# Kernel optimization log

Measured on AMD Instinct MI355X. Metric: run time of the kernel, lower is better.

## Reference

```python
import jax, jax.numpy as jnp
import numpy as np

H = 4  # num_heads


def _ln(x, g, b, eps=1e-5):
    m = x.mean(-1, keepdims=True)
    v = ((x - m) ** 2).mean(-1, keepdims=True)
    return (x - m) / jnp.sqrt(v + eps) * g + b


def setup_inputs() -> dict:
    key = jax.random.key(0)
    ks = jax.random.split(key, 16)
    B, N, M, dQ, dK, dV = 4, 2048, 2048, 128, 128, 128
    s = 0.02
    return {
        "Q": jax.random.normal(ks[0], (B, N, dQ), jnp.float32),
        "K": jax.random.normal(ks[1], (B, M, dK), jnp.float32),
        "adj_mask": jax.random.randint(ks[2], (B, N, M), 0, 2, jnp.int32),
        "Wq": jax.random.normal(ks[3], (dQ, dV), jnp.float32) * s,
        "bq": jnp.zeros((dV,), jnp.float32),
        "Wk": jax.random.normal(ks[4], (dK, dV), jnp.float32) * s,
        "bk": jnp.zeros((dV,), jnp.float32),
        "Wv": jax.random.normal(ks[5], (dK, dV), jnp.float32) * s,
        "bv": jnp.zeros((dV,), jnp.float32),
        "Wr1": jax.random.normal(ks[6], (dV, dV), jnp.float32) * s,
        "br1": jnp.zeros((dV,), jnp.float32),
        "Wr2": jax.random.normal(ks[7], (dV, dV), jnp.float32) * s,
        "br2": jnp.zeros((dV,), jnp.float32),
        "g0": jnp.ones((dV,), jnp.float32),
        "be0": jnp.zeros((dV,), jnp.float32),
        "g1": jnp.ones((dV,), jnp.float32),
        "be1": jnp.zeros((dV,), jnp.float32),
    }


def reference(Q, K, adj_mask, Wq, bq, Wk, bk, Wv, bv, Wr1, br1, Wr2, br2, g0, be0, g1, be1):
    B, N, _ = Q.shape
    M = K.shape[1]
    dV = Wq.shape[1]
    dh = dV // H
    Qp = Q @ Wq + bq   # [B,N,dV]
    Kp = K @ Wk + bk   # [B,M,dV]
    Vp = K @ Wv + bv   # [B,M,dV]
    # torch: split dim_V into H chunks, cat along dim 0 -> head-major [H*B, L, dh]
    def to_heads(x, L):
        return x.reshape(B, L, H, dh).transpose(2, 0, 1, 3).reshape(H * B, L, dh)
    Qh, Kh, Vh = to_heads(Qp, N), to_heads(Kp, M), to_heads(Vp, M)
    attn = jnp.einsum('bnd,bmd->bnm', Qh, Kh) / jnp.sqrt(jnp.float32(dh))  # [H*B,N,M]
    # torch repeat_interleave(mask, H, dim=0) gives batch-major order -- faithful
    mask = jnp.repeat(adj_mask, H, axis=0)
    attn = jnp.where(mask == 0, -jnp.inf, attn)
    A = jax.nn.softmax(attn, axis=2)
    O = Qh + jnp.einsum('bnm,bmd->bnd', A, Vh)  # [H*B,N,dh]
    # recombine heads back to [B,N,dV] (intended split(dim=0)/cat(dim=2))
    O = O.reshape(H, B, N, dh).transpose(1, 2, 0, 3).reshape(B, N, dV)
    O = _ln(O, g0, be0)
    O = O + (jax.nn.relu(O @ Wr1 + br1) @ Wr2 + br2)
    return _ln(O, g1, be1)
```

## Files before the change

kernel.cpp:

```cpp
#include <hip/hip_runtime.h>
#include <hip/hip_bf16.h>


typedef short bf16x8 __attribute__((ext_vector_type(8)));
typedef float f32x4 __attribute__((ext_vector_type(4)));

#define BN 4
#define SEQ 2048
#define DIM 128
#define NH 4
#define DH 32
#define ROWS (BN * SEQ)
#define MS 4

static __device__ __forceinline__ unsigned short f2bf(float f) {
    __hip_bfloat16 h = __float2bfloat16(f);
    return *reinterpret_cast<unsigned short*>(&h);
}
static __device__ __forceinline__ float bf2f(unsigned short u) {
    union { unsigned int i; float f; } cv;
    cv.i = ((unsigned int)u) << 16;
    return cv.f;
}
static __device__ __forceinline__ unsigned int pack2bf(float a, float b) {
    return (unsigned int)f2bf(a) | ((unsigned int)f2bf(b) << 16);
}

__global__ __launch_bounds__(256) void proj_prep(
    const float* __restrict__ Q, const float* __restrict__ K,
    const float* __restrict__ bq, const float* __restrict__ bk,
    const float* __restrict__ bv,
    const float* __restrict__ Wq, const float* __restrict__ Wk,
    const float* __restrict__ Wv, const float* __restrict__ W1,
    const float* __restrict__ W2,
    float* __restrict__ Qp, unsigned short* __restrict__ Qb,
    unsigned short* __restrict__ Kb, unsigned short* __restrict__ Vt,
    unsigned short* __restrict__ WT)
{
    __shared__ __align__(16) unsigned char smem[52288];
    const int bx = blockIdx.x;
    const int t = threadIdx.x;

    if (bx >= 768) {
        const float* W = (bx == 768) ? W1 : W2;
        unsigned short* out = WT + (bx - 768) * DIM * DIM;
        for (int i = t; i < DIM * DIM; i += 256) {
            int n = i >> 7, k = i & 127;
            out[i] = f2bf(W[k * DIM + n]);
        }
        return;
    }

    unsigned short (*sW)[136] = (unsigned short(*)[136])smem;
    unsigned short (*sX)[136] = (unsigned short(*)[136])(smem + 34816);
    unsigned short (*sY)[137] = (unsigned short(*)[137])(smem + 43520);

    const int proj = bx >> 8;
    const int rowbase = (bx & 255) * 32;
    const float* X = (proj == 0) ? Q : K;
    const float* W = (proj == 0) ? Wq : (proj == 1) ? Wk : Wv;
    const float* bias = (proj == 0) ? bq : (proj == 1) ? bk : bv;
    const int bidx = rowbase >> 11;
    const int srowbase = rowbase & 2047;

#pragma unroll
    for (int i = 0; i < 16; ++i) {
        int idx = i * 256 + t;
        int k = idx >> 5, n4 = (idx & 31) * 4;
        float4 v = *(const float4*)(W + k * DIM + n4);
        sW[n4 + 0][k] = f2bf(v.x);
        sW[n4 + 1][k] = f2bf(v.y);
        sW[n4 + 2][k] = f2bf(v.z);
        sW[n4 + 3][k] = f2bf(v.w);
    }
#pragma unroll
    for (int i = 0; i < 4; ++i) {
        int idx = i * 256 + t;
        int row = idx >> 5, c4 = (idx & 31) * 4;
        float4 v = *(const float4*)(X + (long)(rowbase + row) * DIM + c4);
        sX[row][c4 + 0] = f2bf(v.x);
        sX[row][c4 + 1] = f2bf(v.y);
        sX[row][c4 + 2] = f2bf(v.z);
        sX[row][c4 + 3] = f2bf(v.w);
    }
    __syncthreads();

    const int w = t >> 6, lane = t & 63;
    const int n16 = lane & 15, quad = lane >> 4;

    f32x4 acc[2][2];
#pragma unroll
    for (int r = 0; r < 2; ++r)
#pragma unroll
        for (int ct = 0; ct < 2; ++ct)
            acc[r][ct] = (f32x4){0.f, 0.f, 0.f, 0.f};

    for (int ks = 0; ks < 4; ++ks) {
        bf16x8 bfrag[2];
#pragma unroll
        for (int ct = 0; ct < 2; ++ct) {
            int ncol = w * 32 + ct * 16 + n16;
            bfrag[ct] = *(const bf16x8*)(&sW[ncol][ks * 32 + quad * 8]);
        }
#pragma unroll
        for (int r = 0; r < 2; ++r) {
            bf16x8 afrag = *(const bf16x8*)(&sX[r * 16 + n16][ks * 32 + quad * 8]);
#pragma unroll
            for (int ct = 0; ct < 2; ++ct)
                acc[r][ct] = __builtin_amdgcn_mfma_f32_16x16x32_bf16(
                    afrag, bfrag[ct], acc[r][ct], 0, 0, 0);
        }
    }

#pragma unroll
    for (int r = 0; r < 2; ++r) {
#pragma unroll
        for (int ct = 0; ct < 2; ++ct) {
            int col = w * 32 + ct * 16 + n16;
            int hh = col >> 5, dd = col & 31;
            float bv_ = bias[col];
#pragma unroll
            for (int i = 0; i < 4; ++i) {
                int lrow = r * 16 + quad * 4 + i;
                int grow = rowbase + lrow;
                int srow = srowbase + lrow;
                float val = acc[r][ct][i] + bv_;
                if (proj == 0) {
                    Qp[(long)grow * DIM + col] = val;
                    Qb[((long)(hh * BN + bidx) * SEQ + srow) * DH + dd]
                        = f2bf(val * 0.17677669529663687f);
                } else if (proj == 1) {
                    Kb[((long)(hh * BN + bidx) * SEQ + srow) * DH + dd] = f2bf(val);
                } else {
                    sY[lrow][col] = f2bf(val);
                }
            }
        }
    }
    if (proj == 2) {
        __syncthreads();
#pragma unroll
        for (int i = 0; i < 16; ++i) {
            int idx = i * 256 + t;
            int c = idx >> 5, m = idx & 31;
            Vt[((long)bidx * DIM + c) * SEQ + srowbase + m] = sY[m][c];
        }
    }
}

__global__ __launch_bounds__(256, 2) void attn_kernel(
    const unsigned short* __restrict__ Qb, const unsigned short* __restrict__ Kb,
    const unsigned short* __restrict__ Vt, const int* __restrict__ adj,
    unsigned short* __restrict__ Opart, float* __restrict__ Lpart)
{
    __shared__ __align__(16) unsigned short sP[4][32][68];

    const int id = blockIdx.x;
    const int combo = id & 15;
    const int qidx = id >> 4;
    const int h = combo >> 2;
    const int sp = combo & 3;
    const int qbase = qidx * 32;
    const int t = threadIdx.x;
    const int b = t >> 6;
    const int lane = t & 63, n16 = lane & 15, quad = lane >> 4;

    const unsigned short* Qh = Qb + ((long)(h * BN + b) * SEQ) * DH + quad * 8;
    const unsigned short* Kp = Kb + ((long)(h * BN + b) * SEQ) * DH + quad * 8;
    const unsigned short* Vp = Vt + ((long)b * DIM + h * DH) * SEQ + quad * 8;
    const int* Mr[2];
#pragma unroll
    for (int r = 0; r < 2; ++r)
        Mr[r] = adj + ((long)h * SEQ + qbase + r * 16 + n16) * SEQ + quad * 4;

    bf16x8 qfrag[2];
#pragma unroll
    for (int r = 0; r < 2; ++r)
        qfrag[r] = *(const bf16x8*)(Qh + (long)(qbase + r * 16 + n16) * DH);

    f32x4 o[2][2];
    float lsum[2];
#pragma unroll
    for (int r = 0; r < 2; ++r) {
#pragma unroll
        for (int ct = 0; ct < 2; ++ct) o[r][ct] = (f32x4){0.f, 0.f, 0.f, 0.f};
        lsum[r] = 0.f;
    }

    bf16x8 kf[2][2];
    int4 mk[2][2][2];
    const int mb0 = sp * 512;

#pragma unroll
    for (int c = 0; c < 2; ++c)
        kf[0][c] = *(const bf16x8*)(Kp + (long)(mb0 + c * 16 + n16) * DH);
#pragma unroll
    for (int r = 0; r < 2; ++r)
#pragma unroll
        for (int c = 0; c < 2; ++c)
            mk[0][r][c] = *(const int4*)(Mr[r] + mb0 + c * 16);

    const f32x4 zero4 = {0.f, 0.f, 0.f, 0.f};

#pragma unroll
    for (int mt = 0; mt < 16; ++mt) {
        const int cur = mt & 1, nxt = cur ^ 1;
        const int mbc = mb0 + mt * 32;
        bf16x8 vf0 = *(const bf16x8*)(Vp + (long)(0 * 16 + n16) * SEQ + mbc);
        bf16x8 vf1 = *(const bf16x8*)(Vp + (long)(1 * 16 + n16) * SEQ + mbc);
        if (mt < 15) {
            const int mb = mbc + 32;
#pragma unroll
            for (int c = 0; c < 2; ++c)
                kf[nxt][c] = *(const bf16x8*)(Kp + (long)(mb + c * 16 + n16) * DH);
#pragma unroll
            for (int r = 0; r < 2; ++r)
#pragma unroll
                for (int c = 0; c < 2; ++c)
                    mk[nxt][r][c] = *(const int4*)(Mr[r] + mb + c * 16);
        }
#pragma unroll
        for (int r = 0; r < 2; ++r) {
            f32x4 st[2];
#pragma unroll
            for (int c = 0; c < 2; ++c)
                st[c] = __builtin_amdgcn_mfma_f32_16x16x32_bf16(
                    kf[cur][c], qfrag[r], zero4, 0, 0, 0);
            float p[2][4];
#pragma unroll
            for (int c = 0; c < 2; ++c) {
                const int* mp = (const int*)&mk[cur][r][c];
#pragma unroll
                for (int i = 0; i < 4; ++i) {
                    float e = __expf(st[c][i]);
                    p[c][i] = mp[i] ? e : 0.f;
                    lsum[r] += p[c][i];
                }
            }
#pragma unroll
            for (int c = 0; c < 2; ++c) {
                uint2 wv;
                wv.x = pack2bf(p[c][0], p[c][1]);
                wv.y = pack2bf(p[c][2], p[c][3]);
                *(uint2*)&sP[b][r * 16 + n16][c * 16 + quad * 4] = wv;
            }
        }
#pragma unroll
        for (int r = 0; r < 2; ++r) {
            bf16x8 pa = *(const bf16x8*)(&sP[b][r * 16 + n16][quad * 8]);
            o[r][0] = __builtin_amdgcn_mfma_f32_16x16x32_bf16(pa, vf0, o[r][0], 0, 0, 0);
            o[r][1] = __builtin_amdgcn_mfma_f32_16x16x32_bf16(pa, vf1, o[r][1], 0, 0, 0);
        }
    }

#pragma unroll
    for (int r = 0; r < 2; ++r) {
        lsum[r] += __shfl_xor(lsum[r], 16, 64);
        lsum[r] += __shfl_xor(lsum[r], 32, 64);
    }

#pragma unroll
    for (int r = 0; r < 2; ++r)
#pragma unroll
        for (int ct = 0; ct < 2; ++ct)
#pragma unroll
            for (int i = 0; i < 4; ++i)
                sP[b][r * 16 + quad * 4 + i][ct * 16 + n16] = f2bf(o[r][ct][i]);
    {
        const uint4 w0 = *(const uint4*)&sP[b][lane >> 1][(lane & 1) * 16];
        const uint4 w1 = *(const uint4*)&sP[b][lane >> 1][(lane & 1) * 16 + 8];
        unsigned short* Ob = Opart
            + ((((long)sp * NH + h) * BN + b) * SEQ + qbase) * 32;
        *(uint4*)(Ob + (long)lane * 16)     = w0;
        *(uint4*)(Ob + (long)lane * 16 + 8) = w1;
    }

    if (quad == 0) {
#pragma unroll
        for (int r = 0; r < 2; ++r)
            Lpart[(((long)sp * BN + b) * NH + h) * SEQ + qbase + r * 16 + n16] = lsum[r];
    }
}

__global__ __launch_bounds__(256) void epi_kernel(
    const float* __restrict__ Qp, const unsigned short* __restrict__ Opart,
    const float* __restrict__ Lpart, const unsigned short* __restrict__ WT,
    const float* __restrict__ br1, const float* __restrict__ br2,
    const float* __restrict__ g0, const float* __restrict__ be0,
    const float* __restrict__ g1, const float* __restrict__ be1,
    float* __restrict__ out)
{
    __shared__ __align__(16) unsigned short sXb[16][136];
    __shared__ __align__(16) unsigned short sHb[16][136];
    __shared__ __align__(16) float sXf[16][132];

    const int rowbase = blockIdx.x * 16;
    const int t = threadIdx.x;
    const int row = t >> 4, col8 = (t & 15) * 8;
    const int grow = rowbase + row;
    const int bidx = grow >> 11;
    const int srow = grow & 2047;
    const int head = col8 >> 5;
    const int dd = col8 & 31;

    {
        float l = 0.f;
#pragma unroll
        for (int s = 0; s < MS; ++s)
            l += Lpart[(((long)s * BN + bidx) * NH + head) * SEQ + srow];
        float linv = 1.f / l;

        float ovf[8];
#pragma unroll
        for (int j = 0; j < 8; ++j) ovf[j] = 0.f;
#pragma unroll
        for (int s = 0; s < MS; ++s) {
            bf16x8 p = *(const bf16x8*)(Opart
                + ((((long)s * NH + head) * BN + bidx) * SEQ + srow) * 32 + dd);
#pragma unroll
            for (int j = 0; j < 8; ++j) ovf[j] += bf2f((unsigned short)p[j]);
        }

        float vals[8];
        float sum = 0.f, ss = 0.f;
#pragma unroll
        for (int j = 0; j < 8; j += 4) {
            float4 qv = *(const float4*)(Qp + (long)grow * DIM + col8 + j);
            vals[j + 0] = qv.x + ovf[j + 0] * linv;
            vals[j + 1] = qv.y + ovf[j + 1] * linv;
            vals[j + 2] = qv.z + ovf[j + 2] * linv;
            vals[j + 3] = qv.w + ovf[j + 3] * linv;
#pragma unroll
            for (int u = 0; u < 4; ++u) { sum += vals[j + u]; ss += vals[j + u] * vals[j + u]; }
        }
        sum += __shfl_xor(sum, 1, 64); sum += __shfl_xor(sum, 2, 64);
        sum += __shfl_xor(sum, 4, 64); sum += __shfl_xor(sum, 8, 64);
        ss  += __shfl_xor(ss, 1, 64);  ss  += __shfl_xor(ss, 2, 64);
        ss  += __shfl_xor(ss, 4, 64);  ss  += __shfl_xor(ss, 8, 64);
        float mean = sum * (1.f / 128.f);
        float var  = ss * (1.f / 128.f) - mean * mean;
        float rstd = rsqrtf(var + 1e-5f);
#pragma unroll
        for (int j = 0; j < 8; ++j) {
            int col = col8 + j;
            float x = (vals[j] - mean) * rstd * g0[col] + be0[col];
            sXf[row][col] = x;
            sXb[row][col] = f2bf(x);
        }
    }
    __syncthreads();

    const int w = t >> 6, lane = t & 63;
    const int n16 = lane & 15, quad = lane >> 4;
    const unsigned short* W1t = WT;
    const unsigned short* W2t = WT + DIM * DIM;

    f32x4 acc[2];
#pragma unroll
    for (int ct = 0; ct < 2; ++ct) acc[ct] = (f32x4){0.f, 0.f, 0.f, 0.f};
    for (int ks = 0; ks < 4; ++ks) {
        bf16x8 afrag = *(const bf16x8*)(&sXb[n16][ks * 32 + quad * 8]);
#pragma unroll
        for (int ct = 0; ct < 2; ++ct) {
            bf16x8 bfrag = *(const bf16x8*)(W1t + (w * 32 + ct * 16 + n16) * DIM + ks * 32 + quad * 8);
            acc[ct] = __builtin_amdgcn_mfma_f32_16x16x32_bf16(afrag, bfrag, acc[ct], 0, 0, 0);
        }
    }
#pragma unroll
    for (int ct = 0; ct < 2; ++ct) {
        int col = w * 32 + ct * 16 + n16;
        float bb = br1[col];
#pragma unroll
        for (int i = 0; i < 4; ++i) {
            float hv = acc[ct][i] + bb;
            sHb[quad * 4 + i][col] = f2bf(fmaxf(hv, 0.f));
        }
    }
    __syncthreads();

    f32x4 acc2[2];
#pragma unroll
    for (int ct = 0; ct < 2; ++ct) acc2[ct] = (f32x4){0.f, 0.f, 0.f, 0.f};
    for (int ks = 0; ks < 4; ++ks) {
        bf16x8 afrag = *(const bf16x8*)(&sHb[n16][ks * 32 + quad * 8]);
#pragma unroll
        for (int ct = 0; ct < 2; ++ct) {
            bf16x8 bfrag = *(const bf16x8*)(W2t + (w * 32 + ct * 16 + n16) * DIM + ks * 32 + quad * 8);
            acc2[ct] = __builtin_amdgcn_mfma_f32_16x16x32_bf16(afrag, bfrag, acc2[ct], 0, 0, 0);
        }
    }
    float yv[2][4];
#pragma unroll
    for (int ct = 0; ct < 2; ++ct) {
        int col = w * 32 + ct * 16 + n16;
        float bb = br2[col];
#pragma unroll
        for (int i = 0; i < 4; ++i)
            yv[ct][i] = acc2[ct][i] + bb + sXf[quad * 4 + i][col];
    }
    __syncthreads();
#pragma unroll
    for (int ct = 0; ct < 2; ++ct) {
        int col = w * 32 + ct * 16 + n16;
#pragma unroll
        for (int i = 0; i < 4; ++i)
            sXf[quad * 4 + i][col] = yv[ct][i];
    }
    __syncthreads();

    {
        float vals[8];
        float sum = 0.f, ss = 0.f;
#pragma unroll
        for (int j = 0; j < 8; ++j) {
            float v = sXf[row][col8 + j];
            vals[j] = v; sum += v; ss += v * v;
        }
        sum += __shfl_xor(sum, 1, 64); sum += __shfl_xor(sum, 2, 64);
        sum += __shfl_xor(sum, 4, 64); sum += __shfl_xor(sum, 8, 64);
        ss  += __shfl_xor(ss, 1, 64);  ss  += __shfl_xor(ss, 2, 64);
        ss  += __shfl_xor(ss, 4, 64);  ss  += __shfl_xor(ss, 8, 64);
        float mean = sum * (1.f / 128.f);
        float var  = ss * (1.f / 128.f) - mean * mean;
        float rstd = rsqrtf(var + 1e-5f);
        float* op = out + (long)grow * DIM + col8;
#pragma unroll
        for (int j = 0; j < 8; j += 4) {
            float4 ov;
            int col = col8 + j;
            ov.x = (vals[j + 0] - mean) * rstd * g1[col + 0] + be1[col + 0];
            ov.y = (vals[j + 1] - mean) * rstd * g1[col + 1] + be1[col + 1];
            ov.z = (vals[j + 2] - mean) * rstd * g1[col + 2] + be1[col + 2];
            ov.w = (vals[j + 3] - mean) * rstd * g1[col + 3] + be1[col + 3];
            *(float4*)(op + j) = ov;
        }
    }
}

extern "C" void kernel_launch(void* const* d_in, const int* in_sizes, int n_in,
                              void* d_out, int out_size, void* d_ws, size_t ws_size,
                              hipStream_t stream) {
    const float* Q   = (const float*)d_in[0];
    const float* K   = (const float*)d_in[1];
    const int*   adj = (const int*)d_in[2];
    const float* Wq  = (const float*)d_in[3];
    const float* bq  = (const float*)d_in[4];
    const float* Wk  = (const float*)d_in[5];
    const float* bk  = (const float*)d_in[6];
    const float* Wv  = (const float*)d_in[7];
    const float* bv  = (const float*)d_in[8];
    const float* Wr1 = (const float*)d_in[9];
    const float* br1 = (const float*)d_in[10];
    const float* Wr2 = (const float*)d_in[11];
    const float* br2 = (const float*)d_in[12];
    const float* g0  = (const float*)d_in[13];
    const float* be0 = (const float*)d_in[14];
    const float* g1  = (const float*)d_in[15];
    const float* be1 = (const float*)d_in[16];
    float* out = (float*)d_out;

    float* Qp             = (float*)d_ws;
    unsigned short* Opart = (unsigned short*)(Qp + (long)ROWS * DIM);
    float* Lpart          = (float*)(Opart + (long)MS * ROWS * DIM);
    unsigned short* Qb    = (unsigned short*)(Lpart + (long)MS * BN * NH * SEQ);
    unsigned short* Kb    = Qb + (long)ROWS * DIM;
    unsigned short* Vt    = Kb + (long)ROWS * DIM;
    unsigned short* WT    = Vt + (long)ROWS * DIM;

    proj_prep<<<770, 256, 0, stream>>>(Q, K, bq, bk, bv, Wq, Wk, Wv, Wr1, Wr2,
                                       Qp, Qb, Kb, Vt, WT);
    attn_kernel<<<1024, 256, 0, stream>>>(Qb, Kb, Vt, adj, Opart, Lpart);
    epi_kernel<<<512, 256, 0, stream>>>(Qp, Opart, Lpart, WT, br1, br2,
                                        g0, be0, g1, be1, out);
}
```

Measured before the change: 197.2 us.

## Preload adjacency mask once per block as LDS bitmask

The attention kernel now reads each block's 32x512 adjacency mask tile once, all threads sharing the work. It packs each 32-int run into a 32-bit word and keeps the words in shared memory. Before, each of the four waves streamed the same int32 mask rows through per-tile double-buffered global loads. This removes that 4x redundant mask traffic and frees registers. The cost is an up-front load phase plus a barrier before the main loop, with no overlap against compute.

```diff
diff --git a/kernel.cpp b/kernel.cpp
--- a/kernel.cpp
+++ b/kernel.cpp
@@ -154,6 +154,7 @@
     unsigned short* __restrict__ Opart, float* __restrict__ Lpart)
 {
     __shared__ __align__(16) unsigned short sP[4][32][68];
+    __shared__ unsigned int sM[32][17];
 
     const int id = blockIdx.x;
     const int combo = id & 15;
@@ -164,14 +165,29 @@
     const int t = threadIdx.x;
     const int b = t >> 6;
     const int lane = t & 63, n16 = lane & 15, quad = lane >> 4;
+    const int mb0 = sp * 512;
+
+#pragma unroll
+    for (int i = 0; i < 2; ++i) {
+        int wid = i * 256 + t;
+        int row = wid >> 4, w = wid & 15;
+        const int4* src = (const int4*)(adj
+            + ((long)h * SEQ + qbase + row) * SEQ + mb0 + w * 32);
+        unsigned int m = 0;
+#pragma unroll
+        for (int j = 0; j < 8; ++j) {
+            int4 v = src[j];
+            m |= (((unsigned)v.x & 1u) << (4 * j))
+               | (((unsigned)v.y & 1u) << (4 * j + 1))
+               | (((unsigned)v.z & 1u) << (4 * j + 2))
+               | (((unsigned)v.w & 1u) << (4 * j + 3));
+        }
+        sM[row][w] = m;
+    }
 
     const unsigned short* Qh = Qb + ((long)(h * BN + b) * SEQ) * DH + quad * 8;
     const unsigned short* Kp = Kb + ((long)(h * BN + b) * SEQ) * DH + quad * 8;
     const unsigned short* Vp = Vt + ((long)b * DIM + h * DH) * SEQ + quad * 8;
-    const int* Mr[2];
-#pragma unroll
-    for (int r = 0; r < 2; ++r)
-        Mr[r] = adj + ((long)h * SEQ + qbase + r * 16 + n16) * SEQ + quad * 4;
 
     bf16x8 qfrag[2];
 #pragma unroll
@@ -188,17 +204,11 @@
     }
 
     bf16x8 kf[2][2];
-    int4 mk[2][2][2];
-    const int mb0 = sp * 512;
-
 #pragma unroll
     for (int c = 0; c < 2; ++c)
         kf[0][c] = *(const bf16x8*)(Kp + (long)(mb0 + c * 16 + n16) * DH);
-#pragma unroll
-    for (int r = 0; r < 2; ++r)
-#pragma unroll
-        for (int c = 0; c < 2; ++c)
-            mk[0][r][c] = *(const int4*)(Mr[r] + mb0 + c * 16);
+
+    __syncthreads();
 
     const f32x4 zero4 = {0.f, 0.f, 0.f, 0.f};
 
@@ -213,11 +223,6 @@
 #pragma unroll
             for (int c = 0; c < 2; ++c)
                 kf[nxt][c] = *(const bf16x8*)(Kp + (long)(mb + c * 16 + n16) * DH);
-#pragma unroll
-            for (int r = 0; r < 2; ++r)
-#pragma unroll
-                for (int c = 0; c < 2; ++c)
-                    mk[nxt][r][c] = *(const int4*)(Mr[r] + mb + c * 16);
         }
 #pragma unroll
         for (int r = 0; r < 2; ++r) {
@@ -226,17 +231,16 @@
             for (int c = 0; c < 2; ++c)
                 st[c] = __builtin_amdgcn_mfma_f32_16x16x32_bf16(
                     kf[cur][c], qfrag[r], zero4, 0, 0, 0);
+            const unsigned int wm = sM[r * 16 + n16][mt];
             float p[2][4];
 #pragma unroll
-            for (int c = 0; c < 2; ++c) {
-                const int* mp = (const int*)&mk[cur][r][c];
+            for (int c = 0; c < 2; ++c)
 #pragma unroll
                 for (int i = 0; i < 4; ++i) {
                     float e = __expf(st[c][i]);
-                    p[c][i] = mp[i] ? e : 0.f;
+                    p[c][i] = ((wm >> (c * 16 + quad * 4 + i)) & 1u) ? e : 0.f;
                     lsum[r] += p[c][i];
                 }
-            }
 #pragma unroll
             for (int c = 0; c < 2; ++c) {
                 uint2 wv;
```

Result: faster. 178.5 us (-9.5%).
